# Optimization experiments

Hardware: AMD Instinct MI355X
Metric: run time of the kernel (lower is better)

The kernel has to match this reference:

```python
import jax, jax.numpy as jnp
import numpy as np

N = 100000      # nodes
E = 1600000     # edges
R = 4           # relations
F = 128         # node feature dim
EMB = 128       # embedding size
HID = 256       # hidden size
B = 1024        # number of (nest, food) queries


def setup_inputs() -> dict:
    key = jax.random.key(0)
    ks = jax.random.split(key, 12)
    s1 = 1.0 / np.sqrt(F)
    s2 = 1.0 / np.sqrt(EMB)
    sf = 1.0 / np.sqrt(2 * EMB)
    return {
        "x": jax.random.normal(ks[0], (N, F), jnp.float32),
        "edge_index": jax.random.randint(ks[1], (2, E), 0, N),
        "edge_type": jax.random.randint(ks[2], (E,), 0, R),
        "nest_idx": jax.random.randint(ks[3], (B,), 0, N),
        "food_idx": jax.random.randint(ks[4], (B,), 0, N),
        "W_rel1": jax.random.normal(ks[5], (R, F, EMB), jnp.float32) * s1,
        "W_root1": jax.random.normal(ks[6], (F, EMB), jnp.float32) * s1,
        "b1": jnp.zeros((EMB,), jnp.float32),
        "W_rel2": jax.random.normal(ks[7], (R, EMB, EMB), jnp.float32) * s2,
        "W_root2": jax.random.normal(ks[8], (EMB, EMB), jnp.float32) * s2,
        "b2": jnp.zeros((EMB,), jnp.float32),
        "W_fc": jax.random.normal(ks[9], (2 * EMB, HID), jnp.float32) * sf,
        "b_fc": jnp.zeros((HID,), jnp.float32),
    }


def rgcn_conv(x, src, dst, etype, W_rel, W_root, b):
    # Per-relation transform of all nodes: [N, R, O]
    h = jnp.einsum('nf,rfo->nro', x, W_rel)
    msgs = h[src, etype]                      # [E, O] gather per edge
    # Mean aggregation per (dst, relation), PyG RGCNConv default
    key = dst * R + etype                     # [E]
    deg = jax.ops.segment_sum(jnp.ones((E,), x.dtype), key, num_segments=N * R)
    norm = 1.0 / jnp.maximum(deg, 1.0)
    out = jax.ops.segment_sum(msgs * norm[key][:, None], dst, num_segments=N)
    return out + x @ W_root + b


def reference(x, edge_index, edge_type, nest_idx, food_idx,
              W_rel1, W_root1, b1, W_rel2, W_root2, b2, W_fc, b_fc):
    src, dst = edge_index[0], edge_index[1]
    h = jax.nn.relu(rgcn_conv(x, src, dst, edge_type, W_rel1, W_root1, b1))
    h = rgcn_conv(h, src, dst, edge_type, W_rel2, W_root2, b2)
    combined = jnp.concatenate([h[nest_idx], h[food_idx]], axis=-1)  # [B, 2*EMB]
    return jax.nn.relu(combined @ W_fc + b_fc)                        # [B, HID]
```

## Files before the change

kernel.cpp:

```cpp
#include <hip/hip_runtime.h>
#include <stdint.h>

#define NN 100000
#define NE 1600000
#define NR 4
#define NK (NN * NR)
#define FD 128
#define KA 512
#define KT 640
#define NQ 1024
#define HIDN 256

#define NB 391
#define BSH 8
#define CAPB 8192
#define EPB 4096
#define NBLK1 ((NE + EPB - 1) / EPB)
#define MPAD 100096

using u16 = unsigned short;
using u32 = unsigned int;
typedef __attribute__((ext_vector_type(8))) __bf16 bf16x8;
typedef __attribute__((ext_vector_type(4))) float f32x4;

__device__ __forceinline__ u16 f2b(float f) {
    u32 u = __builtin_bit_cast(u32, f);
    u32 r = u + 0x7FFFu + ((u >> 16) & 1u);
    return (u16)(r >> 16);
}
__device__ __forceinline__ float b2f_lo(u32 v) { return __builtin_bit_cast(float, v << 16); }
__device__ __forceinline__ float b2f_hi(u32 v) { return __builtin_bit_cast(float, v & 0xFFFF0000u); }
__device__ __forceinline__ u32 pack2(float a, float b) {
    return (u32)f2b(a) | ((u32)f2b(b) << 16);
}
__device__ __forceinline__ void gload_lds16(const void* g, void* l) {
    __builtin_amdgcn_global_load_lds((const __attribute__((address_space(1))) u32*)g,
                                     (__attribute__((address_space(3))) u32*)l, 16, 0, 0);
}

__global__ __launch_bounds__(256) void bucket_scatter(const int* __restrict__ ei,
                                                      const int* __restrict__ et,
                                                      int* __restrict__ bcnt,
                                                      u32* __restrict__ bpack) {
    __shared__ int hist[NB];
    __shared__ int base[NB];
    int t = threadIdx.x;
    for (int i = t; i < NB; i += 256) hist[i] = 0;
    __syncthreads();
    int e0 = blockIdx.x * EPB;
    int rank[16];
    u32 pk[16];
    int bk[16];
#pragma unroll
    for (int j = 0; j < 16; ++j) {
        int e = e0 + j * 256 + t;
        bk[j] = -1;
        if (e < NE) {
            int src = __builtin_nontemporal_load(ei + e);
            int dst = __builtin_nontemporal_load(ei + NE + e);
            int r   = __builtin_nontemporal_load(et + e);
            bk[j] = dst >> BSH;
            pk[j] = (u32)src | ((u32)r << 17) | ((u32)(dst & 255) << 19);
            rank[j] = atomicAdd(&hist[bk[j]], 1);
        }
    }
    __syncthreads();
    for (int i = t; i < NB; i += 256) {
        int h = hist[i];
        base[i] = h ? atomicAdd(&bcnt[i], h) : 0;
    }
    __syncthreads();
#pragma unroll
    for (int j = 0; j < 16; ++j)
        if (bk[j] >= 0) bpack[(size_t)bk[j] * CAPB + base[bk[j]] + rank[j]] = pk[j];
}

__global__ __launch_bounds__(256) void key_scatter(const int* __restrict__ bcnt,
                                                   const u32* __restrict__ bpack,
                                                   int* __restrict__ offs6,
                                                   int* __restrict__ spack) {
    __shared__ int hist[1024];
    __shared__ int sm[256];
    int b = blockIdx.x, t = threadIdx.x;
    int cnt = bcnt[b];
    const u32* seg = bpack + (size_t)b * CAPB;
#pragma unroll
    for (int j = 0; j < 4; ++j) hist[t + j * 256] = 0;
    __syncthreads();
    for (int i = t; i < cnt; i += 256) atomicAdd(&hist[seg[i] >> 17], 1);
    __syncthreads();
    int t4 = t * 4;
    int h0 = hist[t4], h1 = hist[t4 + 1], h2 = hist[t4 + 2], h3 = hist[t4 + 3];
    int s = h0 + h1 + h2 + h3;
    int sp = (s + 7) & ~7;
    sm[t] = sp;
    __syncthreads();
    for (int o2 = 1; o2 < 256; o2 <<= 1) {
        int n = (t >= o2) ? sm[t - o2] : 0;
        __syncthreads();
        sm[t] += n;
        __syncthreads();
    }
    int bas = b * CAPB + sm[t] - sp;
    int e0 = bas, e1 = e0 + h0, e2 = e1 + h1, e3 = e2 + h2, e4 = e3 + h3, eL = bas + sp;
    int node = (b << 8) + t;
    if (node < NN) {
        int* o = offs6 + (size_t)node * 6;
        o[0] = e0; o[1] = e1; o[2] = e2; o[3] = e3; o[4] = e4; o[5] = eL;
    }
    hist[t4] = e0; hist[t4 + 1] = e1; hist[t4 + 2] = e2; hist[t4 + 3] = e3;
    for (int i = e4; i < eL; ++i) spack[i] = NN;
    __syncthreads();
    for (int i = t; i < cnt; i += 256) {
        u32 pk = seg[i];
        int pos = atomicAdd(&hist[pk >> 17], 1);
        spack[pos] = (int)(pk & 0x1FFFFu);
    }
}

__global__ __launch_bounds__(256) void cvt_bf16(const float* __restrict__ in,
                                                u16* __restrict__ outp, int n) {
    int i = blockIdx.x * 256 + threadIdx.x;
    int idx = i * 4;
    if (idx >= n) return;
    float4 v = *(const float4*)(in + idx);
    u32 lo = (u32)f2b(v.x) | ((u32)f2b(v.y) << 16);
    u32 hi = (u32)f2b(v.z) | ((u32)f2b(v.w) << 16);
    *(uint2*)(outp + idx) = make_uint2(lo, hi);
}

__global__ __launch_bounds__(256) void prep_B(const float* __restrict__ Wrel,
                                              const float* __restrict__ Wroot,
                                              u16* __restrict__ Bt) {
    int i = blockIdx.x * 256 + threadIdx.x;
    if (i >= FD * KT) return;
    int k = i % KT;
    int o = i / KT;
    float v = (k < 512) ? Wrel[(size_t)k * FD + o] : Wroot[(size_t)(k - 512) * FD + o];
    Bt[i] = f2b(v);
}

__global__ __launch_bounds__(256) void agg_kernel(const int* __restrict__ offs6,
                                                  const int* __restrict__ spack,
                                                  const u32* __restrict__ fp,
                                                  u16* __restrict__ Aout,
                                                  int rows,
                                                  const int* __restrict__ nest,
                                                  const int* __restrict__ food,
                                                  int qmode,
                                                  int* __restrict__ qnodes) {
    int wid = threadIdx.x >> 6, lane = threadIdx.x & 63;
    int row = blockIdx.x * 4 + wid;
    if (row >= rows) return;
    int node;
    if (qmode) node = (row < NQ) ? nest[row] : food[row - NQ];
    else node = row;
    node = __builtin_amdgcn_readfirstlane(node);
    if (qmode && lane == 0) qnodes[row] = node;

    const int* ob = offs6 + (size_t)node * 6;
    int o0 = __builtin_amdgcn_readfirstlane(ob[0]);
    int o1 = __builtin_amdgcn_readfirstlane(ob[1]);
    int o2 = __builtin_amdgcn_readfirstlane(ob[2]);
    int o3 = __builtin_amdgcn_readfirstlane(ob[3]);
    int o4 = __builtin_amdgcn_readfirstlane(ob[4]);
    int oL = __builtin_amdgcn_readfirstlane(ob[5]);

    float a00 = 0, a01 = 0, a10 = 0, a11 = 0, a20 = 0, a21 = 0, a30 = 0, a31 = 0;

    for (int e = o0; e < oL; e += 8) {
        int p[8];
        u32 v[8];
#pragma unroll
        for (int j = 0; j < 8; ++j)
            p[j] = __builtin_amdgcn_readfirstlane(spack[e + j]);
#pragma unroll
        for (int j = 0; j < 8; ++j) v[j] = fp[(size_t)p[j] * 64 + lane];
#pragma unroll
        for (int j = 0; j < 8; ++j) {
            int ij = e + j;
            float f0 = b2f_lo(v[j]);
            float f1 = b2f_hi(v[j]);
            if (ij < o1)      { a00 += f0; a01 += f1; }
            else if (ij < o2) { a10 += f0; a11 += f1; }
            else if (ij < o3) { a20 += f0; a21 += f1; }
            else              { a30 += f0; a31 += f1; }
        }
    }

    int d0 = o1 - o0, d1 = o2 - o1, d2 = o3 - o2, d3 = o4 - o3;
    float s0 = 1.0f / (float)(d0 > 1 ? d0 : 1);
    float s1 = 1.0f / (float)(d1 > 1 ? d1 : 1);
    float s2 = 1.0f / (float)(d2 > 1 ? d2 : 1);
    float s3 = 1.0f / (float)(d3 > 1 ? d3 : 1);
    u16* Ao = Aout + (size_t)row * KA + lane * 2;
    __builtin_nontemporal_store(pack2(a00 * s0, a01 * s0), (u32*)(Ao + 0));
    __builtin_nontemporal_store(pack2(a10 * s1, a11 * s1), (u32*)(Ao + 128));
    __builtin_nontemporal_store(pack2(a20 * s2, a21 * s2), (u32*)(Ao + 256));
    __builtin_nontemporal_store(pack2(a30 * s3, a31 * s3), (u32*)(Ao + 384));
}

__global__ __launch_bounds__(256) void gemm_lds64(const u16* __restrict__ A,
                                                  const u16* __restrict__ rootSrc,
                                                  const int* __restrict__ rootIdx,
                                                  const u16* __restrict__ Bt,
                                                  const float* __restrict__ bias,
                                                  void* __restrict__ Cout,
                                                  int M, int relu, int outBf16) {
    __shared__ u16 As[2][4096];
    int tid = threadIdx.x;
    int wid = tid >> 6, lane = tid & 63;
    int wm = wid >> 1, wn = wid & 1;
    int lr = lane & 15, hi = lane >> 4;
    int row0 = blockIdx.x * 64;

    f32x4 acc[2][4];
#pragma unroll
    for (int i = 0; i < 2; ++i)
#pragma unroll
        for (int j = 0; j < 4; ++j) acc[i][j] = (f32x4){0.f, 0.f, 0.f, 0.f};

    int srow = wid * 8 + (lane >> 3);
    int sg = (lane & 7) ^ (lane >> 3);

    auto stage = [&](int t, int buf) {
#pragma unroll
        for (int i = 0; i < 2; ++i) {
            int r = i * 32 + srow;
            int gr = row0 + r;
            const u16* src;
            if (t < 8) {
                src = A + (size_t)gr * KA + t * 64 + sg * 8;
            } else {
                int idx = rootIdx ? rootIdx[gr] : gr;
                src = rootSrc + (size_t)idx * FD + (t - 8) * 64 + sg * 8;
            }
            gload_lds16(src, (char*)As[buf] + i * 4096 + wid * 1024);
        }
    };

    stage(0, 0);
    __syncthreads();

    for (int t = 0; t < 10; ++t) {
        int cur = t & 1;
        bf16x8 bfr[2][4];
#pragma unroll
        for (int kk = 0; kk < 2; ++kk)
#pragma unroll
            for (int ni = 0; ni < 4; ++ni) {
                int col = wn * 64 + ni * 16 + lr;
                bfr[kk][ni] = *reinterpret_cast<const bf16x8*>(
                    Bt + (size_t)col * KT + t * 64 + kk * 32 + hi * 8);
            }
        if (t + 1 < 10) stage(t + 1, cur ^ 1);
#pragma unroll
        for (int kk = 0; kk < 2; ++kk) {
            bf16x8 afr[2];
#pragma unroll
            for (int mi = 0; mi < 2; ++mi) {
                int r = wm * 32 + mi * 16 + lr;
                int sp = (kk * 4 + hi) ^ (lr & 7);
                afr[mi] = *reinterpret_cast<const bf16x8*>((char*)As[cur] + r * 128 + sp * 16);
            }
#pragma unroll
            for (int mi = 0; mi < 2; ++mi)
#pragma unroll
                for (int ni = 0; ni < 4; ++ni)
                    acc[mi][ni] = __builtin_amdgcn_mfma_f32_16x16x32_bf16(afr[mi], bfr[kk][ni], acc[mi][ni], 0, 0, 0);
        }
        __syncthreads();
    }

#pragma unroll
    for (int mi = 0; mi < 2; ++mi) {
#pragma unroll
        for (int ni = 0; ni < 4; ++ni) {
            int col = wn * 64 + ni * 16 + lr;
            float bv = bias[col];
#pragma unroll
            for (int rg = 0; rg < 4; ++rg) {
                int row = row0 + wm * 32 + mi * 16 + hi * 4 + rg;
                if (row < M) {
                    float v = acc[mi][ni][rg] + bv;
                    if (relu) v = fmaxf(v, 0.f);
                    if (outBf16) ((u16*)Cout)[(size_t)row * FD + col] = f2b(v);
                    else ((float*)Cout)[(size_t)row * FD + col] = v;
                }
            }
        }
    }
}

__global__ __launch_bounds__(256) void fc_kernel(const float* __restrict__ h2q,
                                                 const float* __restrict__ Wfc,
                                                 const float* __restrict__ bfc,
                                                 float* __restrict__ out) {
    __shared__ float comb[2 * FD];
    int q = blockIdx.x, t = threadIdx.x;
    if (t < FD) comb[t] = h2q[(size_t)q * FD + t];
    else comb[t] = h2q[(size_t)(NQ + q) * FD + (t - FD)];
    __syncthreads();
    float s = bfc[t];
#pragma unroll 4
    for (int k = 0; k < 2 * FD; ++k) s += comb[k] * Wfc[(size_t)k * HIDN + t];
    out[(size_t)q * HIDN + t] = fmaxf(s, 0.f);
}

extern "C" void kernel_launch(void* const* d_in, const int* in_sizes, int n_in,
                              void* d_out, int out_size, void* d_ws, size_t ws_size,
                              hipStream_t stream) {
    const float* x      = (const float*)d_in[0];
    const int*   ei     = (const int*)d_in[1];
    const int*   et     = (const int*)d_in[2];
    const int*   nest   = (const int*)d_in[3];
    const int*   food   = (const int*)d_in[4];
    const float* Wrel1  = (const float*)d_in[5];
    const float* Wroot1 = (const float*)d_in[6];
    const float* b1     = (const float*)d_in[7];
    const float* Wrel2  = (const float*)d_in[8];
    const float* Wroot2 = (const float*)d_in[9];
    const float* b2     = (const float*)d_in[10];
    const float* Wfc    = (const float*)d_in[11];
    const float* bfc    = (const float*)d_in[12];
    float* out = (float*)d_out;

    char* w = (char*)d_ws;
    size_t off = 0;
    auto take = [&](size_t b) {
        char* p = w + off;
        off += b;
        off = (off + 255) & ~(size_t)255;
        return p;
    };
    int* bcnt   = (int*)take((size_t)NB * 4);
    int* offs6  = (int*)take((size_t)NN * 6 * 4);
    u32* bpack  = (u32*)take((size_t)NB * CAPB * 4);
    int* spack  = (int*)take((size_t)NB * CAPB * 4);
    int* qnodes = (int*)take((size_t)2 * NQ * 4);
    u16* xh     = (u16*)take((size_t)MPAD * FD * 2);
    u16* h1     = (u16*)take((size_t)MPAD * FD * 2);
    u16* Bt1    = (u16*)take((size_t)FD * KT * 2);
    u16* Bt2    = (u16*)take((size_t)FD * KT * 2);
    u16* A1     = (u16*)take((size_t)MPAD * KA * 2);
    u16* A2     = (u16*)take((size_t)2 * NQ * KA * 2);
    float* h2q  = (float*)take((size_t)2 * NQ * FD * 4);

    hipMemsetAsync(bcnt, 0, (size_t)NB * 4, stream);
    hipMemsetAsync(xh + (size_t)NN * FD, 0, FD * 2, stream);
    hipMemsetAsync(h1 + (size_t)NN * FD, 0, FD * 2, stream);
    cvt_bf16<<<((NN * FD / 4) + 255) / 256, 256, 0, stream>>>(x, xh, NN * FD);
    prep_B<<<(FD * KT + 255) / 256, 256, 0, stream>>>(Wrel1, Wroot1, Bt1);
    prep_B<<<(FD * KT + 255) / 256, 256, 0, stream>>>(Wrel2, Wroot2, Bt2);
    bucket_scatter<<<NBLK1, 256, 0, stream>>>(ei, et, bcnt, bpack);
    key_scatter<<<NB, 256, 0, stream>>>(bcnt, bpack, offs6, spack);

    agg_kernel<<<(NN + 3) / 4, 256, 0, stream>>>(offs6, spack, (const u32*)xh, A1,
                                                 NN, nullptr, nullptr, 0, nullptr);
    gemm_lds64<<<MPAD / 64, 256, 0, stream>>>(A1, xh, nullptr, Bt1, b1,
                                              (void*)h1, NN, 1, 1);

    agg_kernel<<<(2 * NQ + 3) / 4, 256, 0, stream>>>(offs6, spack, (const u32*)h1, A2,
                                                     2 * NQ, nest, food, 1, qnodes);
    gemm_lds64<<<(2 * NQ) / 64, 256, 0, stream>>>(A2, h1, qnodes, Bt2, b2,
                                                  (void*)h2q, 2 * NQ, 0, 0);
    fc_kernel<<<NQ, 256, 0, stream>>>(h2q, Wfc, bfc, out);
}
```

Measured before the change: 272.6 us.

## Load full-K A tile into LDS once and remove per-step barriers in GEMM

The GEMM now stages the whole 64x640 bf16 A tile (aggregated features plus root features) into LDS with one burst of async global-to-LDS loads and a single barrier, replacing the double-buffered 64-wide K loop that synchronized every step. B fragments are software-prefetched from global one K step ahead in registers. This removes nine barriers and lets all loads overlap, but uses 80 KB LDS per block, which lowers occupancy and removes load/compute overlap within a block.

```diff
diff --git a/kernel.cpp b/kernel.cpp
--- a/kernel.cpp
+++ b/kernel.cpp
@@ -17,6 +17,7 @@
 #define EPB 4096
 #define NBLK1 ((NE + EPB - 1) / EPB)
 #define MPAD 100096
+#define LROWB 1280
 
 using u16 = unsigned short;
 using u32 = unsigned int;
@@ -200,76 +201,71 @@
     __builtin_nontemporal_store(pack2(a30 * s3, a31 * s3), (u32*)(Ao + 384));
 }
 
-__global__ __launch_bounds__(256) void gemm_lds64(const u16* __restrict__ A,
+__global__ __launch_bounds__(256) void gemm_fullk(const u16* __restrict__ A,
                                                   const u16* __restrict__ rootSrc,
                                                   const int* __restrict__ rootIdx,
                                                   const u16* __restrict__ Bt,
                                                   const float* __restrict__ bias,
                                                   void* __restrict__ Cout,
                                                   int M, int relu, int outBf16) {
-    __shared__ u16 As[2][4096];
+    __shared__ u16 As[64 * KT];
+    char* lds = (char*)As;
     int tid = threadIdx.x;
     int wid = tid >> 6, lane = tid & 63;
     int wm = wid >> 1, wn = wid & 1;
     int lr = lane & 15, hi = lane >> 4;
     int row0 = blockIdx.x * 64;
 
+#pragma unroll
+    for (int i = 0; i < 20; ++i) {
+        int b = (wid * 20 + i) * 1024 + lane * 16;
+        int r = b / LROWB;
+        int kb = b - r * LROWB;
+        int kbs = kb ^ ((r & 7) << 4);
+        int gr = row0 + r;
+        int idx = rootIdx ? ((kbs >= 1024) ? rootIdx[gr] : gr) : gr;
+        const char* srcA = (const char*)A + (size_t)gr * (KA * 2) + kbs;
+        const char* srcR = (const char*)rootSrc + (size_t)idx * (FD * 2) + (kbs - 1024);
+        const char* src = (kbs < 1024) ? srcA : srcR;
+        gload_lds16(src, lds + (wid * 20 + i) * 1024);
+    }
+    __syncthreads();
+
     f32x4 acc[2][4];
 #pragma unroll
     for (int i = 0; i < 2; ++i)
 #pragma unroll
         for (int j = 0; j < 4; ++j) acc[i][j] = (f32x4){0.f, 0.f, 0.f, 0.f};
 
-    int srow = wid * 8 + (lane >> 3);
-    int sg = (lane & 7) ^ (lane >> 3);
-
-    auto stage = [&](int t, int buf) {
-#pragma unroll
-        for (int i = 0; i < 2; ++i) {
-            int r = i * 32 + srow;
-            int gr = row0 + r;
-            const u16* src;
-            if (t < 8) {
-                src = A + (size_t)gr * KA + t * 64 + sg * 8;
-            } else {
-                int idx = rootIdx ? rootIdx[gr] : gr;
-                src = rootSrc + (size_t)idx * FD + (t - 8) * 64 + sg * 8;
-            }
-            gload_lds16(src, (char*)As[buf] + i * 4096 + wid * 1024);
-        }
-    };
-
-    stage(0, 0);
-    __syncthreads();
-
-    for (int t = 0; t < 10; ++t) {
-        int cur = t & 1;
-        bf16x8 bfr[2][4];
-#pragma unroll
-        for (int kk = 0; kk < 2; ++kk)
-#pragma unroll
-            for (int ni = 0; ni < 4; ++ni) {
-                int col = wn * 64 + ni * 16 + lr;
-                bfr[kk][ni] = *reinterpret_cast<const bf16x8*>(
-                    Bt + (size_t)col * KT + t * 64 + kk * 32 + hi * 8);
-            }
-        if (t + 1 < 10) stage(t + 1, cur ^ 1);
-#pragma unroll
-        for (int kk = 0; kk < 2; ++kk) {
-            bf16x8 afr[2];
-#pragma unroll
-            for (int mi = 0; mi < 2; ++mi) {
-                int r = wm * 32 + mi * 16 + lr;
-                int sp = (kk * 4 + hi) ^ (lr & 7);
-                afr[mi] = *reinterpret_cast<const bf16x8*>((char*)As[cur] + r * 128 + sp * 16);
-            }
-#pragma unroll
-            for (int mi = 0; mi < 2; ++mi)
-#pragma unroll
-                for (int ni = 0; ni < 4; ++ni)
-                    acc[mi][ni] = __builtin_amdgcn_mfma_f32_16x16x32_bf16(afr[mi], bfr[kk][ni], acc[mi][ni], 0, 0, 0);
-        }
-        __syncthreads();
+    const u16* bp[4];
+#pragma unroll
+    for (int ni = 0; ni < 4; ++ni)
+        bp[ni] = Bt + (size_t)(wn * 64 + ni * 16 + lr) * KT + hi * 8;
+
+    bf16x8 bfr[2][4];
+#pragma unroll
+    for (int ni = 0; ni < 4; ++ni) bfr[0][ni] = *reinterpret_cast<const bf16x8*>(bp[ni]);
+
+#pragma unroll
+    for (int ks = 0; ks < 20; ++ks) {
+        int cur = ks & 1;
+        if (ks + 1 < 20) {
+#pragma unroll
+            for (int ni = 0; ni < 4; ++ni)
+                bfr[cur ^ 1][ni] = *reinterpret_cast<const bf16x8*>(bp[ni] + (ks + 1) * 32);
+        }
+        bf16x8 afr[2];
+#pragma unroll
+        for (int mi = 0; mi < 2; ++mi) {
+            int rr = wm * 32 + mi * 16 + lr;
+            afr[mi] = *reinterpret_cast<const bf16x8*>(
+                lds + rr * LROWB + ((ks * 64 + hi * 16) ^ ((rr & 7) << 4)));
+        }
+#pragma unroll
+        for (int mi = 0; mi < 2; ++mi)
+#pragma unroll
+            for (int ni = 0; ni < 4; ++ni)
+                acc[mi][ni] = __builtin_amdgcn_mfma_f32_16x16x32_bf16(afr[mi], bfr[cur][ni], acc[mi][ni], 0, 0, 0);
     }
 
 #pragma unroll
@@ -357,12 +353,12 @@
 
     agg_kernel<<<(NN + 3) / 4, 256, 0, stream>>>(offs6, spack, (const u32*)xh, A1,
                                                  NN, nullptr, nullptr, 0, nullptr);
-    gemm_lds64<<<MPAD / 64, 256, 0, stream>>>(A1, xh, nullptr, Bt1, b1,
+    gemm_fullk<<<MPAD / 64, 256, 0, stream>>>(A1, xh, nullptr, Bt1, b1,
                                               (void*)h1, NN, 1, 1);
 
     agg_kernel<<<(2 * NQ + 3) / 4, 256, 0, stream>>>(offs6, spack, (const u32*)h1, A2,
                                                      2 * NQ, nest, food, 1, qnodes);
-    gemm_lds64<<<(2 * NQ) / 64, 256, 0, stream>>>(A2, h1, qnodes, Bt2, b2,
+    gemm_fullk<<<(2 * NQ) / 64, 256, 0, stream>>>(A2, h1, qnodes, Bt2, b2,
                                                   (void*)h2q, 2 * NQ, 0, 0);
     fc_kernel<<<NQ, 256, 0, stream>>>(h2q, Wfc, bfc, out);
 }
```

New measurement: 290.0 us. 1.06x slower.
